# Kernel tuning notes

Hardware: AMD Instinct MI355X
Metric: run time of the kernel (lower is better)

The kernel has to match this reference:

```python
import jax, jax.numpy as jnp
import numpy as np

B, T, D = 2, 2048, 1024
F = 4096
E = 8


def setup_inputs() -> dict:
    key = jax.random.key(0)
    k0, k1, k2, k3 = jax.random.split(key, 4)
    x = jax.random.normal(k0, (B, T, D), dtype=jnp.float32)
    Wg = jax.random.normal(k1, (E, D), dtype=jnp.float32) * 0.02   # gate Linear weight [E, D]
    W1 = jax.random.normal(k2, (E, D, F), dtype=jnp.float32) * 0.02  # expert up-proj
    W2 = jax.random.normal(k3, (E, F, D), dtype=jnp.float32) * 0.02  # expert down-proj
    return {"x": x, "Wg": Wg, "W1": W1, "W2": W2}


def reference(x, Wg, W1, W2):
    b, t, d = x.shape
    h = x.reshape(-1, d)                              # [N, D], N = b*t
    # --- top-2 gate ---
    logits = h @ Wg.T                                 # [N, E]
    scores, idx = jax.lax.top_k(logits, 2)            # [N, 2], [N, 2]
    scores = jax.nn.softmax(scores.astype(jnp.float32), axis=-1).astype(x.dtype)
    # --- all-expert dense FFN (SiLU MLP) ---
    up = jnp.einsum('nd,edf->enf', h, W1)             # [E, N, F]
    act = jax.nn.silu(up)
    out = jnp.einsum('enf,efd->ned', act, W2)         # [N, E, D]
    # --- combine top-2 ---
    sel = jnp.take_along_axis(out, idx[:, :, None], axis=1)  # [N, 2, D]
    y = jnp.sum(scores[:, :, None] * sel, axis=1)     # [N, D]
    return y.reshape(b, t, d)
```

## Files before the change

kernel.cpp:

```cpp
#include <hip/hip_runtime.h>
#include <hip/hip_bf16.h>
#include <stdint.h>

#define N_TOK 4096
#define D_DIM 1024
#define F_DIM 4096
#define E_NUM 8

typedef unsigned short u16;
typedef __attribute__((ext_vector_type(8))) short short8;
typedef __attribute__((ext_vector_type(4))) float f32x4;

__device__ __forceinline__ u16 f2bf(float f) {
  union { float f; uint32_t u; } v; v.f = f;
  uint32_t u = v.u;
  uint32_t r = (u + 0x7FFFu + ((u >> 16) & 1u)) >> 16;
  return (u16)r;
}

__device__ __forceinline__ void gld_lds16(const u16* g, u16* l) {
  __builtin_amdgcn_global_load_lds(
      (const __attribute__((address_space(1))) uint32_t*)g,
      (__attribute__((address_space(3))) uint32_t*)l, 16, 0, 0);
}

__global__ __launch_bounds__(256) void prep_kernel(
    const float* __restrict__ x, const float* __restrict__ Wg,
    const float* __restrict__ W1, const float* __restrict__ W2,
    u16* __restrict__ xb, int2* __restrict__ choice, float* __restrict__ sc2,
    u16* __restrict__ w1t, u16* __restrict__ w2t) {
  int bid = blockIdx.x;
  if (bid < 1024) {
    int n = bid * 4 + (threadIdx.x >> 6);
    int l = threadIdx.x & 63;
    const float* xr = x + (size_t)n * D_DIM;
    u16* xbr = xb + (size_t)n * D_DIM;
    float acc[E_NUM];
#pragma unroll
    for (int e = 0; e < E_NUM; ++e) acc[e] = 0.f;
    for (int d = l; d < D_DIM; d += 64) {
      float xv = xr[d];
      xbr[d] = f2bf(xv);
#pragma unroll
      for (int e = 0; e < E_NUM; ++e) acc[e] += xv * Wg[e * D_DIM + d];
    }
#pragma unroll
    for (int e = 0; e < E_NUM; ++e) {
      float v = acc[e];
#pragma unroll
      for (int off = 32; off > 0; off >>= 1) v += __shfl_xor(v, off);
      acc[e] = v;
    }
    if (l == 0) {
      int i0 = 0; float m0 = acc[0];
#pragma unroll
      for (int e = 1; e < E_NUM; ++e) if (acc[e] > m0) { m0 = acc[e]; i0 = e; }
      int i1 = -1; float m1 = -INFINITY;
#pragma unroll
      for (int e = 0; e < E_NUM; ++e) if (e != i0 && acc[e] > m1) { m1 = acc[e]; i1 = e; }
      float z = __expf(m1 - m0);
      float s0 = 1.f / (1.f + z);
      sc2[n * 2 + 0] = s0;
      sc2[n * 2 + 1] = 1.f - s0;
      choice[n] = make_int2(i0, i1);
    }
    return;
  }
  __shared__ u16 tile[64][72];
  const float* src; u16* dst; int R, C, bx, by, e;
  if (bid < 1024 + 8192) {
    int s = bid - 1024; bx = s & 63; by = (s >> 6) & 15; e = s >> 10;
    R = D_DIM; C = F_DIM;
    src = W1 + (size_t)e * R * C; dst = w1t + (size_t)e * R * C;
  } else {
    int s = bid - 1024 - 8192; bx = s & 15; by = (s >> 4) & 63; e = s >> 10;
    R = F_DIM; C = D_DIM;
    src = W2 + (size_t)e * R * C; dst = w2t + (size_t)e * R * C;
  }
  int r0 = by * 64, c0 = bx * 64;
  int tid = threadIdx.x;
  int lr = tid & 15;
  int rr = tid >> 4;
#pragma unroll
  for (int p = 0; p < 4; ++p) {
    int r = rr + p * 16;
    float4 v = *(const float4*)&src[(size_t)(r0 + r) * C + c0 + lr * 4];
    tile[lr * 4 + 0][r] = f2bf(v.x);
    tile[lr * 4 + 1][r] = f2bf(v.y);
    tile[lr * 4 + 2][r] = f2bf(v.z);
    tile[lr * 4 + 3][r] = f2bf(v.w);
  }
  __syncthreads();
#pragma unroll
  for (int p = 0; p < 4; ++p) {
    int c = rr + p * 16;
    ushort4 o = *(const ushort4*)&tile[c][lr * 4];
    *(ushort4*)&dst[(size_t)(c0 + c) * R + r0 + lr * 4] = o;
  }
}

__global__ void route_kernel(const int2* __restrict__ choice, int* __restrict__ cnt,
                             int* __restrict__ tok_list) {
  int e = blockIdx.x;
  int l = threadIdx.x;
  unsigned long long below = (l == 0) ? 0ull : ((~0ull) >> (64 - l));
  int c = 0;
  for (int it = 0; it < N_TOK / 64; ++it) {
    int n = it * 64 + l;
    int2 ch = choice[n];
    unsigned long long b0 = __ballot(ch.x == e);
    if (ch.x == e) tok_list[e * N_TOK + c + __popcll(b0 & below)] = 2 * n;
    c += __popcll(b0);
    unsigned long long b1 = __ballot(ch.y == e);
    if (ch.y == e) tok_list[e * N_TOK + c + __popcll(b1 & below)] = 2 * n + 1;
    c += __popcll(b1);
  }
  if (l == 0) cnt[e] = c;
}

__global__ void prefix_kernel(const int* __restrict__ cnt, int* __restrict__ base) {
  if (threadIdx.x == 0) {
    int s = 0;
    for (int e = 0; e < E_NUM; ++e) { base[e] = s; s += cnt[e]; }
  }
}

__global__ __launch_bounds__(512) void up_gemm(
    const u16* __restrict__ xb, const u16* __restrict__ w1t,
    const int* __restrict__ cnt, const int* __restrict__ base,
    const int* __restrict__ tok_list, u16* __restrict__ act) {
  __shared__ u16 As[2][128 * 32];
  __shared__ u16 Bs[2][128 * 32];

  const int bid = blockIdx.x;
  const int orig = (bid & 7) * 1024 + (bid >> 3);
  const int bx = orig & 31, by = (orig >> 5) & 31, e = orig >> 10;

  const int ce = cnt[e];
  const int row0 = by * 128;
  if (row0 >= ce) return;
  const int col0 = bx * 128;
  const int be = base[e];

  const int tid = threadIdx.x;
  const int wave = tid >> 6, lane = tid & 63;
  const int wm = wave >> 2, wn = wave & 3;
  const int lr = lane & 15, kq = lane >> 4;

  const int rsA = wave * 16 + (lane >> 2);
  const int kb = (((lane & 3) ^ ((lane >> 3) & 3)) * 8);
  const int kq8 = ((kq ^ ((lr >> 1) & 3)) * 8);

  int ga = row0 + rsA;
  int e0 = (ga < ce) ? (tok_list[e * N_TOK + ga] & (2 * N_TOK - 1)) : 0;
  const u16* srcA = xb + (e0 >> 1) * D_DIM + kb;
  const u16* srcB = w1t + (size_t)(e * F_DIM + col0 + rsA) * D_DIM + kb;

  f32x4 acc[4][2];
#pragma unroll
  for (int m = 0; m < 4; ++m)
#pragma unroll
    for (int n = 0; n < 2; ++n) acc[m][n] = (f32x4){0.f, 0.f, 0.f, 0.f};

#define USTAGE(k0, b)                              \
  do {                                             \
    gld_lds16(srcA + (k0), &As[b][wave * 512]);    \
    gld_lds16(srcB + (k0), &Bs[b][wave * 512]);    \
  } while (0)

#define UCOMPUTE(b)                                                           \
  do {                                                                        \
    short8 a[4], bb[2];                                                       \
    _Pragma("unroll") for (int m = 0; m < 4; ++m)                             \
        a[m] = *(const short8*)&As[b][(wm * 64 + m * 16 + lr) * 32 + kq8];    \
    _Pragma("unroll") for (int n = 0; n < 2; ++n)                             \
        bb[n] = *(const short8*)&Bs[b][(wn * 32 + n * 16 + lr) * 32 + kq8];   \
    _Pragma("unroll") for (int m = 0; m < 4; ++m)                             \
        _Pragma("unroll") for (int n = 0; n < 2; ++n)                         \
            acc[m][n] = __builtin_amdgcn_mfma_f32_16x16x32_bf16(a[m], bb[n], acc[m][n], 0, 0, 0); \
  } while (0)

  const int NT = D_DIM / 32;
  USTAGE(0, 0);
  USTAGE(32, 1);
  asm volatile("s_waitcnt vmcnt(2)" ::: "memory");
  __builtin_amdgcn_s_barrier();
  __builtin_amdgcn_sched_barrier(0);
  int cur = 0;
  for (int t = 0; t < NT; ++t) {
    UCOMPUTE(cur);
    __builtin_amdgcn_sched_barrier(0);
    __builtin_amdgcn_s_barrier();
    __builtin_amdgcn_sched_barrier(0);
    if (t + 2 < NT) {
      USTAGE((t + 2) * 32, cur);
      asm volatile("s_waitcnt vmcnt(2)" ::: "memory");
    } else {
      asm volatile("s_waitcnt vmcnt(0)" ::: "memory");
    }
    __builtin_amdgcn_s_barrier();
    __builtin_amdgcn_sched_barrier(0);
    cur ^= 1;
  }
#undef USTAGE
#undef UCOMPUTE

#pragma unroll
  for (int m = 0; m < 4; ++m) {
#pragma unroll
    for (int rg = 0; rg < 4; ++rg) {
      int row = wm * 64 + m * 16 + kq * 4 + rg;
      int i = row0 + row;
      if (i < ce) {
        u16* dst = act + (size_t)(be + i) * F_DIM + col0 + wn * 32;
#pragma unroll
        for (int n = 0; n < 2; ++n) {
          float v = acc[m][n][rg];
          float s = v / (1.f + __expf(-v));
          dst[n * 16 + lr] = f2bf(s);
        }
      }
    }
  }
}

__global__ __launch_bounds__(512) void down_gemm(
    const u16* __restrict__ act, const u16* __restrict__ w2t,
    const int* __restrict__ cnt, const int* __restrict__ base,
    const int* __restrict__ tok_list, const float* __restrict__ sc2,
    float* __restrict__ out) {
  __shared__ u16 As[2][128 * 32];
  __shared__ u16 Bs[2][128 * 32];
  __shared__ int toks[128];

  const int bid = blockIdx.x;
  const int orig = (bid & 7) * 256 + (bid >> 3);
  const int bx = orig & 7, by = (orig >> 3) & 31, e = orig >> 8;

  const int ce = cnt[e];
  const int row0 = by * 128;
  if (row0 >= ce) return;
  const int col0 = bx * 128;
  const int be = base[e];

  const int tid = threadIdx.x;
  const int wave = tid >> 6, lane = tid & 63;
  const int wm = wave >> 2, wn = wave & 3;
  const int lr = lane & 15, kq = lane >> 4;

  if (tid < 128) {
    int i = row0 + tid;
    toks[tid] = (i < ce) ? tok_list[e * N_TOK + i] : -1;
  }
  __syncthreads();

  const int rsA = wave * 16 + (lane >> 2);
  const int kb = (((lane & 3) ^ ((lane >> 3) & 3)) * 8);
  const int kq8 = ((kq ^ ((lr >> 1) & 3)) * 8);

  int ra = min(be + row0 + rsA, 2 * N_TOK - 1);
  const u16* srcA = act + (size_t)ra * F_DIM + kb;
  const u16* srcB = w2t + (size_t)(e * D_DIM + col0 + rsA) * F_DIM + kb;

  f32x4 acc[4][2];
#pragma unroll
  for (int m = 0; m < 4; ++m)
#pragma unroll
    for (int n = 0; n < 2; ++n) acc[m][n] = (f32x4){0.f, 0.f, 0.f, 0.f};

#define DSTAGE(k0, b)                              \
  do {                                             \
    gld_lds16(srcA + (k0), &As[b][wave * 512]);    \
    gld_lds16(srcB + (k0), &Bs[b][wave * 512]);    \
  } while (0)

#define DCOMPUTE(b)                                                           \
  do {                                                                        \
    short8 a[4], bb[2];                                                       \
    _Pragma("unroll") for (int m = 0; m < 4; ++m)                             \
        a[m] = *(const short8*)&As[b][(wm * 64 + m * 16 + lr) * 32 + kq8];    \
    _Pragma("unroll") for (int n = 0; n < 2; ++n)                             \
        bb[n] = *(const short8*)&Bs[b][(wn * 32 + n * 16 + lr) * 32 + kq8];   \
    _Pragma("unroll") for (int m = 0; m < 4; ++m)                             \
        _Pragma("unroll") for (int n = 0; n < 2; ++n)                         \
            acc[m][n] = __builtin_amdgcn_mfma_f32_16x16x32_bf16(a[m], bb[n], acc[m][n], 0, 0, 0); \
  } while (0)

  const int NT = F_DIM / 32;
  DSTAGE(0, 0);
  DSTAGE(32, 1);
  asm volatile("s_waitcnt vmcnt(2)" ::: "memory");
  __builtin_amdgcn_s_barrier();
  __builtin_amdgcn_sched_barrier(0);
  int cur = 0;
  for (int t = 0; t < NT; ++t) {
    DCOMPUTE(cur);
    __builtin_amdgcn_sched_barrier(0);
    __builtin_amdgcn_s_barrier();
    __builtin_amdgcn_sched_barrier(0);
    if (t + 2 < NT) {
      DSTAGE((t + 2) * 32, cur);
      asm volatile("s_waitcnt vmcnt(2)" ::: "memory");
    } else {
      asm volatile("s_waitcnt vmcnt(0)" ::: "memory");
    }
    __builtin_amdgcn_s_barrier();
    __builtin_amdgcn_sched_barrier(0);
    cur ^= 1;
  }
#undef DSTAGE
#undef DCOMPUTE

#pragma unroll
  for (int m = 0; m < 4; ++m) {
#pragma unroll
    for (int rg = 0; rg < 4; ++rg) {
      int row = wm * 64 + m * 16 + kq * 4 + rg;
      int ent = toks[row];
      if (ent >= 0) {
        int tokn = ent >> 1;
        float sc = sc2[tokn * 2 + (ent & 1)];
        float* dst = out + (size_t)tokn * D_DIM + col0 + wn * 32;
#pragma unroll
        for (int n = 0; n < 2; ++n)
          atomicAdd(&dst[n * 16 + lr], acc[m][n][rg] * sc);
      }
    }
  }
}

extern "C" void kernel_launch(void* const* d_in, const int* in_sizes, int n_in,
                              void* d_out, int out_size, void* d_ws, size_t ws_size,
                              hipStream_t stream) {
  const float* x  = (const float*)d_in[0];
  const float* Wg = (const float*)d_in[1];
  const float* W1 = (const float*)d_in[2];
  const float* W2 = (const float*)d_in[3];
  float* out = (float*)d_out;

  char* ws = (char*)d_ws;
  size_t off = 0;
  u16* xb  = (u16*)(ws + off); off += (size_t)N_TOK * D_DIM * 2;
  u16* w1t = (u16*)(ws + off); off += (size_t)E_NUM * F_DIM * D_DIM * 2;
  u16* w2t = (u16*)(ws + off); off += (size_t)E_NUM * D_DIM * F_DIM * 2;
  u16* act = (u16*)(ws + off); off += (size_t)2 * N_TOK * F_DIM * 2;
  int* tok_list = (int*)(ws + off); off += (size_t)E_NUM * N_TOK * 4;
  float* sc2 = (float*)(ws + off); off += (size_t)N_TOK * 2 * 4;
  int2* choice = (int2*)(ws + off); off += (size_t)N_TOK * 8;
  int* cnt  = (int*)(ws + off); off += 128;
  int* base = (int*)(ws + off); off += 128;

  hipMemsetAsync(d_out, 0, (size_t)out_size * 4, stream);

  prep_kernel<<<dim3(1024 + 16384), 256, 0, stream>>>(x, Wg, W1, W2, xb, choice,
                                                      sc2, w1t, w2t);
  route_kernel<<<E_NUM, 64, 0, stream>>>(choice, cnt, tok_list);
  prefix_kernel<<<1, 1, 0, stream>>>(cnt, base);

  up_gemm<<<dim3(8192), 512, 0, stream>>>(xb, w1t, cnt, base, tok_list, act);
  down_gemm<<<dim3(2048), 512, 0, stream>>>(act, w2t, cnt, base, tok_list, sc2, out);
}
```

Before: 320.2 us.

## Move W2 transpose-convert into up_gemm launch to overlap with expert GEMM

Removes the W2 fp32-to-bf16 transpose from prep_kernel and runs it as extra leading blocks in the up_gemm launch, using a shared LDS buffer. The W2 conversion can then overlap with the up-projection GEMM blocks rather than serialising before routing. The transpose tile is also reshaped to 64x128 per 512-thread block with vectorised ushort4/uint4 LDS and global stores. The cost is a larger, heterogeneous up_gemm grid, which may interfere with GEMM block scheduling and cache use.

Result: no change. 314.7 us, median of 2 (-1.7%).

```diff
diff --git a/kernel.cpp b/kernel.cpp
--- a/kernel.cpp
+++ b/kernel.cpp
@@ -26,9 +26,9 @@
 
 __global__ __launch_bounds__(256) void prep_kernel(
     const float* __restrict__ x, const float* __restrict__ Wg,
-    const float* __restrict__ W1, const float* __restrict__ W2,
+    const float* __restrict__ W1,
     u16* __restrict__ xb, int2* __restrict__ choice, float* __restrict__ sc2,
-    u16* __restrict__ w1t, u16* __restrict__ w2t) {
+    u16* __restrict__ w1t) {
   int bid = blockIdx.x;
   if (bid < 1024) {
     int n = bid * 4 + (threadIdx.x >> 6);
@@ -67,16 +67,11 @@
     return;
   }
   __shared__ u16 tile[64][72];
-  const float* src; u16* dst; int R, C, bx, by, e;
-  if (bid < 1024 + 8192) {
-    int s = bid - 1024; bx = s & 63; by = (s >> 6) & 15; e = s >> 10;
-    R = D_DIM; C = F_DIM;
-    src = W1 + (size_t)e * R * C; dst = w1t + (size_t)e * R * C;
-  } else {
-    int s = bid - 1024 - 8192; bx = s & 15; by = (s >> 4) & 63; e = s >> 10;
-    R = F_DIM; C = D_DIM;
-    src = W2 + (size_t)e * R * C; dst = w2t + (size_t)e * R * C;
-  }
+  int s = bid - 1024;
+  int bx = s & 63, by = (s >> 6) & 15, e = s >> 10;
+  const int R = D_DIM, C = F_DIM;
+  const float* src = W1 + (size_t)e * R * C;
+  u16* dst = w1t + (size_t)e * R * C;
   int r0 = by * 64, c0 = bx * 64;
   int tid = threadIdx.x;
   int lr = tid & 15;
@@ -127,13 +122,56 @@
 
 __global__ __launch_bounds__(512) void up_gemm(
     const u16* __restrict__ xb, const u16* __restrict__ w1t,
+    const float* __restrict__ W2, u16* __restrict__ w2t,
     const int* __restrict__ cnt, const int* __restrict__ base,
     const int* __restrict__ tok_list, u16* __restrict__ act) {
-  __shared__ u16 As[2][128 * 32];
-  __shared__ u16 Bs[2][128 * 32];
+  __shared__ u16 smem[16384];
 
   const int bid = blockIdx.x;
-  const int orig = (bid & 7) * 1024 + (bid >> 3);
+  if (bid < 4096) {
+    u16 (*tile)[72] = (u16(*)[72])smem;
+    int s = bid;
+    int bx = s & 7, by = (s >> 3) & 63, e = s >> 9;
+    const int R = F_DIM, C = D_DIM;
+    const float* src = W2 + (size_t)e * R * C;
+    u16* dst = w2t + (size_t)e * R * C;
+    int r0 = by * 64, c0 = bx * 128;
+    int tid = threadIdx.x;
+    {
+      int sc = tid & 31, sr = tid >> 5;
+      const float* b0p = &src[(size_t)(r0 + sr * 4) * C + c0 + sc * 4];
+      float4 v0 = *(const float4*)(b0p + 0 * C);
+      float4 v1 = *(const float4*)(b0p + 1 * C);
+      float4 v2 = *(const float4*)(b0p + 2 * C);
+      float4 v3 = *(const float4*)(b0p + 3 * C);
+      ushort4 w;
+      w.x = f2bf(v0.x); w.y = f2bf(v1.x); w.z = f2bf(v2.x); w.w = f2bf(v3.x);
+      *(ushort4*)&tile[sc * 4 + 0][sr * 4] = w;
+      w.x = f2bf(v0.y); w.y = f2bf(v1.y); w.z = f2bf(v2.y); w.w = f2bf(v3.y);
+      *(ushort4*)&tile[sc * 4 + 1][sr * 4] = w;
+      w.x = f2bf(v0.z); w.y = f2bf(v1.z); w.z = f2bf(v2.z); w.w = f2bf(v3.z);
+      *(ushort4*)&tile[sc * 4 + 2][sr * 4] = w;
+      w.x = f2bf(v0.w); w.y = f2bf(v1.w); w.z = f2bf(v2.w); w.w = f2bf(v3.w);
+      *(ushort4*)&tile[sc * 4 + 3][sr * 4] = w;
+    }
+    __syncthreads();
+    {
+      int c = tid >> 2, rq = tid & 3;
+      u16* dp = &dst[(size_t)(c0 + c) * R + r0 + rq * 16];
+      const u16* tp = &tile[c][rq * 16];
+      uint4 a0 = *(const uint4*)(tp + 0);
+      uint4 a1 = *(const uint4*)(tp + 8);
+      *(uint4*)(dp + 0) = a0;
+      *(uint4*)(dp + 8) = a1;
+    }
+    return;
+  }
+
+  u16 (*As)[4096] = (u16(*)[4096])smem;
+  u16 (*Bs)[4096] = (u16(*)[4096])(smem + 8192);
+
+  const int ubid = bid - 4096;
+  const int orig = (ubid & 7) * 1024 + (ubid >> 3);
   const int bx = orig & 31, by = (orig >> 5) & 31, e = orig >> 10;
 
   const int ce = cnt[e];
@@ -352,11 +390,12 @@
 
   hipMemsetAsync(d_out, 0, (size_t)out_size * 4, stream);
 
-  prep_kernel<<<dim3(1024 + 16384), 256, 0, stream>>>(x, Wg, W1, W2, xb, choice,
-                                                      sc2, w1t, w2t);
+  prep_kernel<<<dim3(1024 + 8192), 256, 0, stream>>>(x, Wg, W1, xb, choice,
+                                                     sc2, w1t);
   route_kernel<<<E_NUM, 64, 0, stream>>>(choice, cnt, tok_list);
   prefix_kernel<<<1, 1, 0, stream>>>(cnt, base);
 
-  up_gemm<<<dim3(8192), 512, 0, stream>>>(xb, w1t, cnt, base, tok_list, act);
+  up_gemm<<<dim3(4096 + 8192), 512, 0, stream>>>(xb, w1t, W2, w2t, cnt, base,
+                                                 tok_list, act);
   down_gemm<<<dim3(2048), 512, 0, stream>>>(act, w2t, cnt, base, tok_list, sc2, out);
 }
```
